# Performance work log

Measured on AMD Instinct MI355X. Metric: run time of the kernel, lower is better.

The kernel has to match this reference:

```python
import jax, jax.numpy as jnp
import numpy as np
from jax import lax

ALIGNED_H = 7
ALIGNED_W = 7
SPATIAL_SCALE = 0.125
B, C, H, W = 4, 512, 96, 96
R = 512
IMG = 768  # image resolution (features are image/8)


def setup_inputs() -> dict:
    key = jax.random.key(0)
    k1, k2, k3, k4, k5, k6 = jax.random.split(key, 6)
    features = jax.random.normal(k1, (B, C, H, W), dtype=jnp.float32)
    # realistic rois: [batch_idx, x1, y1, x2, y2] in image coordinates
    bi = jax.random.randint(k2, (R,), 0, B).astype(jnp.float32)
    cx = jax.random.uniform(k3, (R,), minval=32.0, maxval=float(IMG - 32))
    cy = jax.random.uniform(k4, (R,), minval=32.0, maxval=float(IMG - 32))
    bw = jax.random.uniform(k5, (R,), minval=16.0, maxval=256.0)
    bh = jax.random.uniform(k6, (R,), minval=16.0, maxval=256.0)
    x1 = jnp.clip(cx - bw / 2, 0.0, IMG - 1.0)
    x2 = jnp.clip(cx + bw / 2, 0.0, IMG - 1.0)
    y1 = jnp.clip(cy - bh / 2, 0.0, IMG - 1.0)
    y2 = jnp.clip(cy + bh / 2, 0.0, IMG - 1.0)
    rois = jnp.stack([bi, x1, y1, x2, y2], axis=1)
    return {"features": features, "rois": rois}


def _roi_align_ada(features, rois, ah, aw, scale):
    """RoIAlignAda: per output pixel, average of a 3x3 adaptive-stride grid of
    bilinear samples centered at the bin point (RT-MDNet ROIAlignAdaForward)."""
    b, c, h, w = features.shape
    r = rois.shape[0]
    batch_ind = rois[:, 0].astype(jnp.int32)
    x1 = rois[:, 1] * scale
    y1 = rois[:, 2] * scale
    x2 = rois[:, 3] * scale
    y2 = rois[:, 4] * scale
    roi_w = jnp.maximum(x2 - x1, 0.0)
    roi_h = jnp.maximum(y2 - y1, 0.0)
    bin_h = roi_h / (ah - 1.0)  # [R]
    bin_w = roi_w / (aw - 1.0)
    ph = jnp.arange(ah, dtype=jnp.float32)
    pw = jnp.arange(aw, dtype=jnp.float32)
    hc = y1[:, None] + ph[None, :] * bin_h[:, None]  # [R, AH] bin centers
    wc = x1[:, None] + pw[None, :] * bin_w[:, None]  # [R, AW]
    stride_h = jnp.maximum(1.0, jnp.round(bin_h / 3.0))  # [R]
    stride_w = jnp.maximum(1.0, jnp.round(bin_w / 3.0))

    center_ok = ((hc >= 0) & (hc < h))[:, :, None] & ((wc >= 0) & (wc < w))[:, None, :]  # [R,AH,AW]

    # flatten spatial for gathers: [B*H*W, C]
    f = features.transpose(0, 2, 3, 1).reshape(b * h * w, c)
    base = batch_ind[:, None, None] * (h * w)  # [R,1,1]

    acc = jnp.zeros((r, ah, aw, c), dtype=features.dtype)
    cnt = jnp.zeros((r, ah, aw), dtype=features.dtype)
    for sh in (-1.0, 0.0, 1.0):
        for sw in (-1.0, 0.0, 1.0):
            ch = hc + sh * stride_h[:, None]  # [R,AH]
            cw = wc + sw * stride_w[:, None]  # [R,AW]
            valid = ((ch >= 0) & (ch < h))[:, :, None] & ((cw >= 0) & (cw < w))[:, None, :]
            hs = jnp.clip(jnp.floor(ch), 0.0, h - 2.0)
            ws = jnp.clip(jnp.floor(cw), 0.0, w - 2.0)
            hr = (ch - hs)[:, :, None]  # [R,AH,1]
            wr = (cw - ws)[:, None, :] * jnp.ones((r, ah, aw), features.dtype)[:, :1, :1]  # broadcast helper
            wr = (cw - ws)[:, None, :]  # [R,1,AW]
            hsi = hs.astype(jnp.int32)[:, :, None]  # [R,AH,1]
            wsi = ws.astype(jnp.int32)[:, None, :]  # [R,1,AW]
            ul = base + hsi * w + wsi  # [R,AH,AW]
            v = (f[ul] * ((1.0 - hr) * (1.0 - wr))[..., None]
                 + f[ul + 1] * ((1.0 - hr) * wr)[..., None]
                 + f[ul + w] * (hr * (1.0 - wr))[..., None]
                 + f[ul + w + 1] * (hr * wr)[..., None])  # [R,AH,AW,C]
            acc = acc + jnp.where(valid[..., None], v, 0.0)
            cnt = cnt + valid.astype(features.dtype)

    out = jnp.where(center_ok[..., None], acc / jnp.maximum(cnt, 1.0)[..., None], 0.0)
    return out.transpose(0, 3, 1, 2)  # [R, C, AH, AW]


def reference(features, rois):
    x = _roi_align_ada(features, rois, ALIGNED_H + 4, ALIGNED_W + 4, SPATIAL_SCALE)  # [R,C,11,11]
    # fused 3x3 stride-2 max pool -> [R, C, 5, 5]
    out = lax.reduce_window(x, -jnp.inf, lax.max,
                            window_dimensions=(1, 1, 3, 3),
                            window_strides=(1, 1, 2, 2),
                            padding='VALID')
    return out
```

## Files before the change

### kernel.cpp

```cpp
#include <hip/hip_runtime.h>
#include <stdint.h>

typedef unsigned short u16;
typedef unsigned int   u32;

#define Bn 4
#define Cc 512
#define Hh 96
#define Ww 96
#define HWc (Hh*Ww)
#define AH 11
#define Rr 512
#define CP (Cc/2)

__device__ __forceinline__ u16 f2bf(float f){
  u32 u = __float_as_uint(f);
  u += 0x7fffu + ((u>>16)&1u);
  return (u16)(u>>16);
}
__device__ __forceinline__ u32 pk2(float a, float b){
  return (u32)f2bf(a) | ((u32)f2bf(b)<<16);
}

__global__ __launch_bounds__(256)
void transpose_kernel(const float* __restrict__ in, u32* __restrict__ out){
  __shared__ u32 tile[128*64];
  const int t = threadIdx.x;
  const int hw0 = blockIdx.x*128, c0 = blockIdx.y*128, b = blockIdx.z;
  {
    const int q = t & 31, cp0 = t >> 5;
    const float* ib = in + ((size_t)(b*Cc + c0))*HWc + hw0 + 4*q;
    #pragma unroll
    for (int p=0;p<8;++p){
      const int cp = cp0 + p*8;
      const float* pa = ib + (size_t)(2*cp)*HWc;
      float4 A = *(const float4*)pa;
      float4 B = *(const float4*)(pa + HWc);
      const int cs = cp ^ q;
      tile[(4*q+0)*64 + cs] = pk2(A.x,B.x);
      tile[(4*q+1)*64 + cs] = pk2(A.y,B.y);
      tile[(4*q+2)*64 + cs] = pk2(A.z,B.z);
      tile[(4*q+3)*64 + cs] = pk2(A.w,B.w);
    }
  }
  __syncthreads();
  {
    const int l = t & 63, wv = t >> 6;
    u32* ob = out + ((size_t)b*HWc + hw0)*CP + (c0>>1) + l;
    #pragma unroll
    for (int k=0;k<32;++k){
      const int hw = wv*32 + k;
      ob[(size_t)hw*CP] = tile[hw*64 + (l ^ (hw>>2))];
    }
  }
}

__global__ __launch_bounds__(128)
void roi_align_max_nhwc(const u32* __restrict__ feat,
                        const float* __restrict__ rois,
                        float* __restrict__ out)
{
  __shared__ __align__(16) int4   s_ro[AH];
  __shared__ __align__(16) float4 s_rw[AH];
  __shared__ __align__(16) int4   s_co[AH];
  __shared__ __align__(16) float4 s_cw[AH];
  __shared__ int s_b;
  __shared__ __align__(16) float s_out[256*25];

  const int t    = threadIdx.x;
  const int r    = blockIdx.x >> 1;
  const int half = blockIdx.x & 1;

  if (t == 0){
    int b = (int)rois[r*5+0];
    s_b = min(max(b, 0), Bn-1);
  }

  if (t < AH || (t >= 64 && t < 64+AH)){
    const bool isrow = (t < AH);
    const int  p = isrow ? t : t-64;
    const float* rp = rois + r*5;
    const float c1 = rp[isrow?2:1], c2 = rp[isrow?4:3];
    float lo  = __fmul_rn(c1, 0.125f);
    float hi  = __fmul_rn(c2, 0.125f);
    float ext = fmaxf(__fsub_rn(hi,lo), 0.0f);
    float bin = __fdiv_rn(ext, 10.0f);
    float ctr = __fadd_rn(lo, __fmul_rn((float)p, bin));
    float strd = fmaxf(1.0f, rintf(__fdiv_rn(bin, 3.0f)));
    bool ok = (ctr >= 0.0f) && (ctr < 96.0f);
    int rws[6]; float wts[6]; int nv=0;
    #pragma unroll
    for (int s=0;s<3;++s){
      float cc = __fadd_rn(ctr, __fmul_rn((float)(s-1), strd));
      bool vv = (cc >= 0.0f) && (cc < 96.0f);
      float fl = fminf(fmaxf(floorf(cc),0.0f),94.0f);
      float fr = __fsub_rn(cc, fl);
      int ri = (int)fl;
      rws[2*s]=ri; rws[2*s+1]=ri+1;
      wts[2*s]  = vv ? __fsub_rn(1.0f,fr) : 0.0f;
      wts[2*s+1]= vv ? fr : 0.0f;
      nv += vv?1:0;
    }
    float sc = ok ? (1.0f/(float)nv) : 0.0f;
    int cr[4]={0,0,0,0}; float cwv[4]={0.0f,0.0f,0.0f,0.0f}; int n=0;
    for (int k=0;k<6;++k){
      float wk=wts[k]; if (wk==0.0f) continue;
      int rr=rws[k]; bool fnd=false;
      for (int j=0;j<n;++j) if (cr[j]==rr){ cwv[j]+=wk; fnd=true; break; }
      if (!fnd && n<4){ cr[n]=rr; cwv[n]=wk; ++n; }
    }
    const int mul = isrow ? (Ww*CP) : CP;
    if (isrow){
      s_ro[p] = make_int4(cr[0]*mul, cr[1]*mul, cr[2]*mul, cr[3]*mul);
      s_rw[p] = make_float4(cwv[0]*sc, cwv[1]*sc, cwv[2]*sc, cwv[3]*sc);
    } else {
      s_co[p] = make_int4(cr[0]*mul, cr[1]*mul, cr[2]*mul, cr[3]*mul);
      s_cw[p] = make_float4(cwv[0]*sc, cwv[1]*sc, cwv[2]*sc, cwv[3]*sc);
    }
  }
  __syncthreads();

  const u32* fbase = feat + (size_t)s_b*((size_t)HWc*CP);
  const int tb = half*128 + t;

  int   vo[AH][4]; float cwr[AH][4];
  #pragma unroll
  for (int pw=0; pw<AH; ++pw){
    int4 c4 = s_co[pw]; float4 w4 = s_cw[pw];
    vo[pw][0]=tb+c4.x; vo[pw][1]=tb+c4.y; vo[pw][2]=tb+c4.z; vo[pw][3]=tb+c4.w;
    cwr[pw][0]=w4.x; cwr[pw][1]=w4.y; cwr[pw][2]=w4.z; cwr[pw][3]=w4.w;
  }

  float2 awin[5];
  #pragma unroll 1
  for (int ph=0; ph<AH; ++ph){
    int4   r4 = s_ro[ph];
    float4 w4 = s_rw[ph];
    const u32* r0 = fbase + __builtin_amdgcn_readfirstlane(r4.x);
    const u32* r1 = fbase + __builtin_amdgcn_readfirstlane(r4.y);
    const u32* r2 = fbase + __builtin_amdgcn_readfirstlane(r4.z);
    const u32* r3 = fbase + __builtin_amdgcn_readfirstlane(r4.w);
    const float rw_[4] = {w4.x, w4.y, w4.z, w4.w};
    float2 binr[AH];
    #pragma unroll
    for (int pw=0; pw<AH; ++pw){
      u32 v[16];
      #pragma unroll
      for (int j=0;j<4;++j){
        v[0*4+j] = r0[vo[pw][j]];
        v[1*4+j] = r1[vo[pw][j]];
        v[2*4+j] = r2[vo[pw][j]];
        v[3*4+j] = r3[vo[pw][j]];
      }
      float ax=0.0f, ay=0.0f;
      #pragma unroll
      for (int i=0;i<4;++i){
        float cx=0.0f, cy=0.0f;
        #pragma unroll
        for (int j=0;j<4;++j){
          u32 d = v[i*4+j];
          cx = fmaf(cwr[pw][j], __uint_as_float(d<<16),           cx);
          cy = fmaf(cwr[pw][j], __uint_as_float(d & 0xffff0000u), cy);
        }
        ax = fmaf(rw_[i], cx, ax);
        ay = fmaf(rw_[i], cy, ay);
      }
      binr[pw] = make_float2(ax, ay);
    }
    float2 rm[5];
    #pragma unroll
    for (int ox=0; ox<5; ++ox){
      rm[ox].x = fmaxf(fmaxf(binr[2*ox].x, binr[2*ox+1].x), binr[2*ox+2].x);
      rm[ox].y = fmaxf(fmaxf(binr[2*ox].y, binr[2*ox+1].y), binr[2*ox+2].y);
    }
    if (ph == 0){
      #pragma unroll
      for (int ox=0; ox<5; ++ox) awin[ox] = rm[ox];
    } else if (ph & 1){
      #pragma unroll
      for (int ox=0; ox<5; ++ox){
        awin[ox].x = fmaxf(awin[ox].x, rm[ox].x);
        awin[ox].y = fmaxf(awin[ox].y, rm[ox].y);
      }
    } else {
      const int oy = (ph-2) >> 1;
      #pragma unroll
      for (int ox=0; ox<5; ++ox){
        s_out[(2*t  )*25 + oy*5 + ox] = fmaxf(awin[ox].x, rm[ox].x);
        s_out[(2*t+1)*25 + oy*5 + ox] = fmaxf(awin[ox].y, rm[ox].y);
        awin[ox] = rm[ox];
      }
    }
  }
  __syncthreads();

  float4* dst = (float4*)(out + (size_t)r*(Cc*25) + half*(256*25));
  const float4* src = (const float4*)s_out;
  for (int k=t; k<(256*25)/4; k+=128) dst[k]=src[k];
}

__global__ __launch_bounds__(512, 1)
void roi_align_max_nchw(const float* __restrict__ feat,
                        const float* __restrict__ rois,
                        float* __restrict__ out)
{
  __shared__ int   s_roff[AH][6];
  __shared__ float s_rw  [AH][6];
  __shared__ int   s_coff[AH][6];
  __shared__ float s_cw  [AH][6];
  __shared__ int   s_b;
  __shared__ __align__(16) float s_out[Cc*25];

  const int t = threadIdx.x;
  const int r = blockIdx.x;

  if (t < AH*6){
    ((float*)s_rw)[t] = 0.0f;  ((int*)s_roff)[t] = 0;
    ((float*)s_cw)[t] = 0.0f;  ((int*)s_coff)[t] = 0;
  }
  if (t == 0){
    int b = (int)rois[r*5+0];
    s_b = min(max(b, 0), Bn-1);
  }
  __syncthreads();

  if (t < AH || (t >= 64 && t < 64+AH)){
    const bool isrow = (t < AH);
    const int  p = isrow ? t : t-64;
    const float* rp = rois + r*5;
    const float c1 = rp[isrow?2:1], c2 = rp[isrow?4:3];
    float lo  = __fmul_rn(c1, 0.125f);
    float hi  = __fmul_rn(c2, 0.125f);
    float ext = fmaxf(__fsub_rn(hi,lo), 0.0f);
    float bin = __fdiv_rn(ext, 10.0f);
    float ctr = __fadd_rn(lo, __fmul_rn((float)p, bin));
    float strd = fmaxf(1.0f, rintf(__fdiv_rn(bin, 3.0f)));
    bool ok = (ctr >= 0.0f) && (ctr < 96.0f);
    int rws[6]; float wts[6]; int nv=0;
    #pragma unroll
    for (int s=0;s<3;++s){
      float cc = __fadd_rn(ctr, __fmul_rn((float)(s-1), strd));
      bool vv = (cc >= 0.0f) && (cc < 96.0f);
      float fl = fminf(fmaxf(floorf(cc),0.0f),94.0f);
      float fr = __fsub_rn(cc, fl);
      int ri = (int)fl;
      rws[2*s]=ri; rws[2*s+1]=ri+1;
      wts[2*s]  = vv ? __fsub_rn(1.0f,fr) : 0.0f;
      wts[2*s+1]= vv ? fr : 0.0f;
      nv += vv?1:0;
    }
    float sc = ok ? (1.0f/(float)nv) : 0.0f;
    int cr[6]; float cw[6]; int n=0;
    for (int k=0;k<6;++k){
      float wk=wts[k]; if (wk==0.0f) continue;
      if (n>0 && cr[n-1]==rws[k]) cw[n-1]+=wk;
      else { cr[n]=rws[k]; cw[n]=wk; ++n; }
    }
    const int mul = isrow ? Ww : 1;
    for (int k=0;k<n;++k){
      int off = cr[k]*mul;
      float wv = cw[k]*sc;
      if (isrow){ s_roff[p][k]=off; s_rw[p][k]=wv; }
      else      { s_coff[p][k]=off; s_cw[p][k]=wv; }
    }
  }
  __syncthreads();

  const float* f0 = feat + ((size_t)s_b*Cc + t)*HWc;
  float awin[5];
  for (int ph=0; ph<AH; ++ph){
    float binrow[AH];
    #pragma unroll
    for (int pw=0; pw<AH; ++pw){
      float acc = 0.0f;
      #pragma unroll
      for (int ai=0; ai<6; ++ai){
        float ra = s_rw[ph][ai];
        if (ra == 0.0f) continue;
        int ro = s_roff[ph][ai];
        #pragma unroll
        for (int bi=0; bi<6; ++bi){
          float cb = s_cw[pw][bi];
          if (cb == 0.0f) continue;
          acc = fmaf(ra*cb, f0[ro + s_coff[pw][bi]], acc);
        }
      }
      binrow[pw] = acc;
    }
    float rm[5];
    #pragma unroll
    for (int ox=0; ox<5; ++ox)
      rm[ox] = fmaxf(fmaxf(binrow[2*ox], binrow[2*ox+1]), binrow[2*ox+2]);
    if (ph == 0){
      #pragma unroll
      for (int ox=0; ox<5; ++ox) awin[ox] = rm[ox];
    } else if (ph & 1){
      #pragma unroll
      for (int ox=0; ox<5; ++ox) awin[ox] = fmaxf(awin[ox], rm[ox]);
    } else {
      int oy = (ph-2) >> 1;
      #pragma unroll
      for (int ox=0; ox<5; ++ox){
        s_out[t*25 + oy*5 + ox] = fmaxf(awin[ox], rm[ox]);
        awin[ox] = rm[ox];
      }
    }
  }
  __syncthreads();

  float4* dst = (float4*)(out + (size_t)r*(Cc*25));
  const float4* src = (const float4*)s_out;
  for (int k=t; k<(Cc*25)/4; k+=512) dst[k]=src[k];
}

extern "C" void kernel_launch(void* const* d_in, const int* in_sizes, int n_in,
                              void* d_out, int out_size, void* d_ws, size_t ws_size,
                              hipStream_t stream)
{
  (void)in_sizes; (void)n_in; (void)out_size;
  const float* feat = (const float*)d_in[0];
  const float* rois = (const float*)d_in[1];
  float* out = (float*)d_out;
  const size_t need = (size_t)Bn*HWc*Cc*sizeof(u16);
  if (ws_size >= need){
    u32* ws = (u32*)d_ws;
    dim3 g(HWc/128, Cc/128, Bn);
    transpose_kernel<<<g, 256, 0, stream>>>(feat, ws);
    roi_align_max_nhwc<<<Rr*2, 128, 0, stream>>>(ws, rois, out);
  } else {
    roi_align_max_nchw<<<Rr, 512, 0, stream>>>(feat, rois, out);
  }
}
```

Baseline: 173.6 us.

## Split RoI row loop across two thread halves with shared-memory merge

Doubles the block to 256 threads so two halves each process about half of the 11 sample rows for the same channel pair. The pooled output row spanning the split is merged through a small shared buffer after an extra barrier. Address arithmetic switches to byte offsets to simplify load addressing. This shortens each thread's serial dependent chain and adds more waves for latency hiding, at the cost of an additional sync and register pressure under the tighter launch bound.

```diff
diff --git a/kernel.cpp b/kernel.cpp
--- a/kernel.cpp
+++ b/kernel.cpp
@@ -55,7 +55,7 @@
   }
 }
 
-__global__ __launch_bounds__(128)
+__global__ __launch_bounds__(256, 4)
 void roi_align_max_nhwc(const u32* __restrict__ feat,
                         const float* __restrict__ rois,
                         float* __restrict__ out)
@@ -65,9 +65,12 @@
   __shared__ __align__(16) int4   s_co[AH];
   __shared__ __align__(16) float4 s_cw[AH];
   __shared__ int s_b;
+  __shared__ __align__(16) float2 s_part[128][5];
   __shared__ __align__(16) float s_out[256*25];
 
   const int t    = threadIdx.x;
+  const int sub  = t >> 7;
+  const int tl   = t & 127;
   const int r    = blockIdx.x >> 1;
   const int half = blockIdx.x & 1;
 
@@ -121,25 +124,27 @@
   __syncthreads();
 
   const u32* fbase = feat + (size_t)s_b*((size_t)HWc*CP);
-  const int tb = half*128 + t;
+  const int tb = half*128 + tl;
 
   int   vo[AH][4]; float cwr[AH][4];
   #pragma unroll
   for (int pw=0; pw<AH; ++pw){
     int4 c4 = s_co[pw]; float4 w4 = s_cw[pw];
-    vo[pw][0]=tb+c4.x; vo[pw][1]=tb+c4.y; vo[pw][2]=tb+c4.z; vo[pw][3]=tb+c4.w;
+    vo[pw][0]=(tb+c4.x)*4; vo[pw][1]=(tb+c4.y)*4; vo[pw][2]=(tb+c4.z)*4; vo[pw][3]=(tb+c4.w)*4;
     cwr[pw][0]=w4.x; cwr[pw][1]=w4.y; cwr[pw][2]=w4.z; cwr[pw][3]=w4.w;
   }
 
-  float2 awin[5];
+  float2 awin[5], rm6s[5];
+  const int ph0 = sub ? 6 : 0;
+  const int phN = sub ? 10 : 5;
   #pragma unroll 1
-  for (int ph=0; ph<AH; ++ph){
+  for (int ph=ph0; ph<=phN; ++ph){
     int4   r4 = s_ro[ph];
     float4 w4 = s_rw[ph];
-    const u32* r0 = fbase + __builtin_amdgcn_readfirstlane(r4.x);
-    const u32* r1 = fbase + __builtin_amdgcn_readfirstlane(r4.y);
-    const u32* r2 = fbase + __builtin_amdgcn_readfirstlane(r4.z);
-    const u32* r3 = fbase + __builtin_amdgcn_readfirstlane(r4.w);
+    const char* r0 = (const char*)(fbase + __builtin_amdgcn_readfirstlane(r4.x));
+    const char* r1 = (const char*)(fbase + __builtin_amdgcn_readfirstlane(r4.y));
+    const char* r2 = (const char*)(fbase + __builtin_amdgcn_readfirstlane(r4.z));
+    const char* r3 = (const char*)(fbase + __builtin_amdgcn_readfirstlane(r4.w));
     const float rw_[4] = {w4.x, w4.y, w4.z, w4.w};
     float2 binr[AH];
     #pragma unroll
@@ -147,10 +152,10 @@
       u32 v[16];
       #pragma unroll
       for (int j=0;j<4;++j){
-        v[0*4+j] = r0[vo[pw][j]];
-        v[1*4+j] = r1[vo[pw][j]];
-        v[2*4+j] = r2[vo[pw][j]];
-        v[3*4+j] = r3[vo[pw][j]];
+        v[0*4+j] = *(const u32*)(r0 + vo[pw][j]);
+        v[1*4+j] = *(const u32*)(r1 + vo[pw][j]);
+        v[2*4+j] = *(const u32*)(r2 + vo[pw][j]);
+        v[3*4+j] = *(const u32*)(r3 + vo[pw][j]);
       }
       float ax=0.0f, ay=0.0f;
       #pragma unroll
@@ -173,9 +178,12 @@
       rm[ox].x = fmaxf(fmaxf(binr[2*ox].x, binr[2*ox+1].x), binr[2*ox+2].x);
       rm[ox].y = fmaxf(fmaxf(binr[2*ox].y, binr[2*ox+1].y), binr[2*ox+2].y);
     }
-    if (ph == 0){
-      #pragma unroll
-      for (int ox=0; ox<5; ++ox) awin[ox] = rm[ox];
+    if (ph == ph0){
+      #pragma unroll
+      for (int ox=0; ox<5; ++ox){
+        awin[ox] = rm[ox];
+        if (sub) rm6s[ox] = rm[ox];
+      }
     } else if (ph & 1){
       #pragma unroll
       for (int ox=0; ox<5; ++ox){
@@ -186,17 +194,30 @@
       const int oy = (ph-2) >> 1;
       #pragma unroll
       for (int ox=0; ox<5; ++ox){
-        s_out[(2*t  )*25 + oy*5 + ox] = fmaxf(awin[ox].x, rm[ox].x);
-        s_out[(2*t+1)*25 + oy*5 + ox] = fmaxf(awin[ox].y, rm[ox].y);
+        s_out[(2*tl  )*25 + oy*5 + ox] = fmaxf(awin[ox].x, rm[ox].x);
+        s_out[(2*tl+1)*25 + oy*5 + ox] = fmaxf(awin[ox].y, rm[ox].y);
         awin[ox] = rm[ox];
       }
+    }
+  }
+  if (!sub){
+    #pragma unroll
+    for (int ox=0; ox<5; ++ox) s_part[tl][ox] = awin[ox];
+  }
+  __syncthreads();
+  if (sub){
+    #pragma unroll
+    for (int ox=0; ox<5; ++ox){
+      float2 p = s_part[tl][ox];
+      s_out[(2*tl  )*25 + 2*5 + ox] = fmaxf(p.x, rm6s[ox].x);
+      s_out[(2*tl+1)*25 + 2*5 + ox] = fmaxf(p.y, rm6s[ox].y);
     }
   }
   __syncthreads();
 
   float4* dst = (float4*)(out + (size_t)r*(Cc*25) + half*(256*25));
   const float4* src = (const float4*)s_out;
-  for (int k=t; k<(256*25)/4; k+=128) dst[k]=src[k];
+  for (int k=t; k<(256*25)/4; k+=256) dst[k]=src[k];
 }
 
 __global__ __launch_bounds__(512, 1)
@@ -326,7 +347,7 @@
     u32* ws = (u32*)d_ws;
     dim3 g(HWc/128, Cc/128, Bn);
     transpose_kernel<<<g, 256, 0, stream>>>(feat, ws);
-    roi_align_max_nhwc<<<Rr*2, 128, 0, stream>>>(ws, rois, out);
+    roi_align_max_nhwc<<<Rr*2, 256, 0, stream>>>(ws, rois, out);
   } else {
     roi_align_max_nchw<<<Rr, 512, 0, stream>>>(feat, rois, out);
   }
```

Measured after the change: 272.3 us. 1.57x slower.

## Split ROI output rows across two block groups and process sample-row pairs

Applied to the files above, without the earlier changes.

Doubles the grid so each ROI/channel-half is handled by two blocks: one computes output rows 0-2 (sample rows 0-6) and the other rows 3-4 (sample rows 6-10). It recomputes the shared boundary sample row, processes two sample rows per iteration with a streaming column max, and switches to byte offsets with column offsets read from LDS instead of held in registers. The aim is more parallelism and lower register pressure for better occupancy. The cost is redundant loads of the overlap rows and a strided, less coalesced output store.

```diff
diff --git a/kernel.cpp b/kernel.cpp
--- a/kernel.cpp
+++ b/kernel.cpp
@@ -55,6 +55,23 @@
   }
 }
 
+__device__ __forceinline__ float2 bilin(const u32 v[16], const float cw[4], const float rw[4]){
+  float ax=0.0f, ay=0.0f;
+  #pragma unroll
+  for (int i=0;i<4;++i){
+    float cx=0.0f, cy=0.0f;
+    #pragma unroll
+    for (int j=0;j<4;++j){
+      u32 d = v[i*4+j];
+      cx = fmaf(cw[j], __uint_as_float(d<<16),           cx);
+      cy = fmaf(cw[j], __uint_as_float(d & 0xffff0000u), cy);
+    }
+    ax = fmaf(rw[i], cx, ax);
+    ay = fmaf(rw[i], cy, ay);
+  }
+  return make_float2(ax, ay);
+}
+
 __global__ __launch_bounds__(128)
 void roi_align_max_nhwc(const u32* __restrict__ feat,
                         const float* __restrict__ rois,
@@ -65,11 +82,14 @@
   __shared__ __align__(16) int4   s_co[AH];
   __shared__ __align__(16) float4 s_cw[AH];
   __shared__ int s_b;
-  __shared__ __align__(16) float s_out[256*25];
+  __shared__ __align__(16) float s_out[256*15];
 
   const int t    = threadIdx.x;
-  const int r    = blockIdx.x >> 1;
-  const int half = blockIdx.x & 1;
+  const int bid  = blockIdx.x;
+  const int rg   = bid >> 10;
+  const int rem  = bid & 1023;
+  const int r    = rem >> 1;
+  const int half = rem & 1;
 
   if (t == 0){
     int b = (int)rois[r*5+0];
@@ -109,7 +129,7 @@
       for (int j=0;j<n;++j) if (cr[j]==rr){ cwv[j]+=wk; fnd=true; break; }
       if (!fnd && n<4){ cr[n]=rr; cwv[n]=wk; ++n; }
     }
-    const int mul = isrow ? (Ww*CP) : CP;
+    const int mul = isrow ? (Ww*CP*4) : (CP*4);
     if (isrow){
       s_ro[p] = make_int4(cr[0]*mul, cr[1]*mul, cr[2]*mul, cr[3]*mul);
       s_rw[p] = make_float4(cwv[0]*sc, cwv[1]*sc, cwv[2]*sc, cwv[3]*sc);
@@ -120,83 +140,119 @@
   }
   __syncthreads();
 
-  const u32* fbase = feat + (size_t)s_b*((size_t)HWc*CP);
-  const int tb = half*128 + t;
-
-  int   vo[AH][4]; float cwr[AH][4];
-  #pragma unroll
-  for (int pw=0; pw<AH; ++pw){
-    int4 c4 = s_co[pw]; float4 w4 = s_cw[pw];
-    vo[pw][0]=tb+c4.x; vo[pw][1]=tb+c4.y; vo[pw][2]=tb+c4.z; vo[pw][3]=tb+c4.w;
-    cwr[pw][0]=w4.x; cwr[pw][1]=w4.y; cwr[pw][2]=w4.z; cwr[pw][3]=w4.w;
-  }
+  const char* fb = (const char*)(feat + (size_t)s_b*((size_t)HWc*CP));
+  const int tb4 = (half*128 + t)*4;
 
   float2 awin[5];
+  const int base  = rg ? 6 : 0;
+  const int NFULL = rg ? 2 : 3;
+
   #pragma unroll 1
-  for (int ph=0; ph<AH; ++ph){
-    int4   r4 = s_ro[ph];
-    float4 w4 = s_rw[ph];
-    const u32* r0 = fbase + __builtin_amdgcn_readfirstlane(r4.x);
-    const u32* r1 = fbase + __builtin_amdgcn_readfirstlane(r4.y);
-    const u32* r2 = fbase + __builtin_amdgcn_readfirstlane(r4.z);
-    const u32* r3 = fbase + __builtin_amdgcn_readfirstlane(r4.w);
-    const float rw_[4] = {w4.x, w4.y, w4.z, w4.w};
-    float2 binr[AH];
+  for (int pp=0; pp<NFULL; ++pp){
+    const int pa = base + 2*pp;
+    int4   ra4 = s_ro[pa];   float4 wa4 = s_rw[pa];
+    int4   rb4 = s_ro[pa+1]; float4 wb4 = s_rw[pa+1];
+    const char* ra0 = fb + __builtin_amdgcn_readfirstlane(ra4.x);
+    const char* ra1 = fb + __builtin_amdgcn_readfirstlane(ra4.y);
+    const char* ra2 = fb + __builtin_amdgcn_readfirstlane(ra4.z);
+    const char* ra3 = fb + __builtin_amdgcn_readfirstlane(ra4.w);
+    const char* rb0 = fb + __builtin_amdgcn_readfirstlane(rb4.x);
+    const char* rb1 = fb + __builtin_amdgcn_readfirstlane(rb4.y);
+    const char* rb2 = fb + __builtin_amdgcn_readfirstlane(rb4.z);
+    const char* rb3 = fb + __builtin_amdgcn_readfirstlane(rb4.w);
+    const float rwa[4] = {wa4.x, wa4.y, wa4.z, wa4.w};
+    const float rwb[4] = {wb4.x, wb4.y, wb4.z, wb4.w};
+    float2 bpp_a = make_float2(0.f,0.f), bp_a = bpp_a;
+    float2 bpp_b = bpp_a, bp_b = bpp_a;
     #pragma unroll
     for (int pw=0; pw<AH; ++pw){
-      u32 v[16];
+      int4 c4 = s_co[pw]; float4 w4 = s_cw[pw];
+      const int oo[4] = {tb4 + c4.x, tb4 + c4.y, tb4 + c4.z, tb4 + c4.w};
+      const float cwv[4] = {w4.x, w4.y, w4.z, w4.w};
+      u32 va[16], vb[16];
       #pragma unroll
       for (int j=0;j<4;++j){
-        v[0*4+j] = r0[vo[pw][j]];
-        v[1*4+j] = r1[vo[pw][j]];
-        v[2*4+j] = r2[vo[pw][j]];
-        v[3*4+j] = r3[vo[pw][j]];
-      }
-      float ax=0.0f, ay=0.0f;
-      #pragma unroll
-      for (int i=0;i<4;++i){
-        float cx=0.0f, cy=0.0f;
-        #pragma unroll
-        for (int j=0;j<4;++j){
-          u32 d = v[i*4+j];
-          cx = fmaf(cwr[pw][j], __uint_as_float(d<<16),           cx);
-          cy = fmaf(cwr[pw][j], __uint_as_float(d & 0xffff0000u), cy);
+        va[0*4+j] = *(const u32*)(ra0 + oo[j]);
+        va[1*4+j] = *(const u32*)(ra1 + oo[j]);
+        va[2*4+j] = *(const u32*)(ra2 + oo[j]);
+        va[3*4+j] = *(const u32*)(ra3 + oo[j]);
+        vb[0*4+j] = *(const u32*)(rb0 + oo[j]);
+        vb[1*4+j] = *(const u32*)(rb1 + oo[j]);
+        vb[2*4+j] = *(const u32*)(rb2 + oo[j]);
+        vb[3*4+j] = *(const u32*)(rb3 + oo[j]);
+      }
+      float2 ca = bilin(va, cwv, rwa);
+      float2 cb = bilin(vb, cwv, rwb);
+      if (pw >= 2 && !(pw & 1)){
+        const int ox = (pw-2) >> 1;
+        float2 rma, rmb;
+        rma.x = fmaxf(fmaxf(bpp_a.x, bp_a.x), ca.x);
+        rma.y = fmaxf(fmaxf(bpp_a.y, bp_a.y), ca.y);
+        rmb.x = fmaxf(fmaxf(bpp_b.x, bp_b.x), cb.x);
+        rmb.y = fmaxf(fmaxf(bpp_b.y, bp_b.y), cb.y);
+        if (pp == 0){
+          awin[ox] = rma;
+        } else {
+          s_out[(2*t  )*15 + (pp-1)*5 + ox] = fmaxf(awin[ox].x, rma.x);
+          s_out[(2*t+1)*15 + (pp-1)*5 + ox] = fmaxf(awin[ox].y, rma.y);
+          awin[ox] = rma;
         }
-        ax = fmaf(rw_[i], cx, ax);
-        ay = fmaf(rw_[i], cy, ay);
-      }
-      binr[pw] = make_float2(ax, ay);
-    }
-    float2 rm[5];
-    #pragma unroll
-    for (int ox=0; ox<5; ++ox){
-      rm[ox].x = fmaxf(fmaxf(binr[2*ox].x, binr[2*ox+1].x), binr[2*ox+2].x);
-      rm[ox].y = fmaxf(fmaxf(binr[2*ox].y, binr[2*ox+1].y), binr[2*ox+2].y);
-    }
-    if (ph == 0){
-      #pragma unroll
-      for (int ox=0; ox<5; ++ox) awin[ox] = rm[ox];
-    } else if (ph & 1){
-      #pragma unroll
-      for (int ox=0; ox<5; ++ox){
-        awin[ox].x = fmaxf(awin[ox].x, rm[ox].x);
-        awin[ox].y = fmaxf(awin[ox].y, rm[ox].y);
-      }
-    } else {
-      const int oy = (ph-2) >> 1;
-      #pragma unroll
-      for (int ox=0; ox<5; ++ox){
-        s_out[(2*t  )*25 + oy*5 + ox] = fmaxf(awin[ox].x, rm[ox].x);
-        s_out[(2*t+1)*25 + oy*5 + ox] = fmaxf(awin[ox].y, rm[ox].y);
-        awin[ox] = rm[ox];
-      }
-    }
-  }
-  __syncthreads();
-
-  float4* dst = (float4*)(out + (size_t)r*(Cc*25) + half*(256*25));
-  const float4* src = (const float4*)s_out;
-  for (int k=t; k<(256*25)/4; k+=128) dst[k]=src[k];
+        awin[ox].x = fmaxf(awin[ox].x, rmb.x);
+        awin[ox].y = fmaxf(awin[ox].y, rmb.y);
+      }
+      bpp_a = bp_a; bp_a = ca;
+      bpp_b = bp_b; bp_b = cb;
+    }
+  }
+
+  {
+    const int pa = base + 2*NFULL;
+    int4   ra4 = s_ro[pa]; float4 wa4 = s_rw[pa];
+    const char* ra0 = fb + __builtin_amdgcn_readfirstlane(ra4.x);
+    const char* ra1 = fb + __builtin_amdgcn_readfirstlane(ra4.y);
+    const char* ra2 = fb + __builtin_amdgcn_readfirstlane(ra4.z);
+    const char* ra3 = fb + __builtin_amdgcn_readfirstlane(ra4.w);
+    const float rwa[4] = {wa4.x, wa4.y, wa4.z, wa4.w};
+    float2 bpp_a = make_float2(0.f,0.f), bp_a = bpp_a;
+    #pragma unroll
+    for (int pw=0; pw<AH; ++pw){
+      int4 c4 = s_co[pw]; float4 w4 = s_cw[pw];
+      const int oo[4] = {tb4 + c4.x, tb4 + c4.y, tb4 + c4.z, tb4 + c4.w};
+      const float cwv[4] = {w4.x, w4.y, w4.z, w4.w};
+      u32 va[16];
+      #pragma unroll
+      for (int j=0;j<4;++j){
+        va[0*4+j] = *(const u32*)(ra0 + oo[j]);
+        va[1*4+j] = *(const u32*)(ra1 + oo[j]);
+        va[2*4+j] = *(const u32*)(ra2 + oo[j]);
+        va[3*4+j] = *(const u32*)(ra3 + oo[j]);
+      }
+      float2 ca = bilin(va, cwv, rwa);
+      if (pw >= 2 && !(pw & 1)){
+        const int ox = (pw-2) >> 1;
+        float2 rma;
+        rma.x = fmaxf(fmaxf(bpp_a.x, bp_a.x), ca.x);
+        rma.y = fmaxf(fmaxf(bpp_a.y, bp_a.y), ca.y);
+        s_out[(2*t  )*15 + (NFULL-1)*5 + ox] = fmaxf(awin[ox].x, rma.x);
+        s_out[(2*t+1)*15 + (NFULL-1)*5 + ox] = fmaxf(awin[ox].y, rma.y);
+      }
+      bpp_a = bp_a; bp_a = ca;
+    }
+  }
+  __syncthreads();
+
+  float* ob = out + (size_t)r*(Cc*25) + half*(256*25);
+  if (rg == 0){
+    for (int k=t; k<256*15; k+=128){
+      int c = k/15, e = k - c*15;
+      ob[c*25 + e] = s_out[k];
+    }
+  } else {
+    for (int k=t; k<256*10; k+=128){
+      int c = k/10, e = k - c*10;
+      ob[c*25 + 15 + e] = s_out[c*15 + e];
+    }
+  }
 }
 
 __global__ __launch_bounds__(512, 1)
@@ -326,7 +382,7 @@
     u32* ws = (u32*)d_ws;
     dim3 g(HWc/128, Cc/128, Bn);
     transpose_kernel<<<g, 256, 0, stream>>>(feat, ws);
-    roi_align_max_nhwc<<<Rr*2, 128, 0, stream>>>(ws, rois, out);
+    roi_align_max_nhwc<<<Rr*4, 128, 0, stream>>>(ws, rois, out);
   } else {
     roi_align_max_nchw<<<Rr, 512, 0, stream>>>(feat, rois, out);
   }
```

New measurement: 229.5 us. 32.2% more time.
